# Performance work log

Hardware: AMD Instinct MI355X
Metric: run time of the kernel (lower is better)

## Reference

```python
import jax, jax.numpy as jnp
import numpy as np

B, N, P, D, NH, DFFN = 4, 1024, 128, 512, 8, 2048
DH = D // NH  # 64


def setup_inputs() -> dict:
    key = jax.random.key(0)
    ks = jax.random.split(key, 64)
    i = [0]
    def rn(shape, s=1.0):
        k = ks[i[0]]; i[0] += 1
        return jax.random.normal(k, shape, jnp.float32) * s
    w = 0.05  # weight init scale
    inp = {
        "H": rn((B, N, D)),
        "V": rn((B, N, 3, D)),
        "D_batch": rn((B, N, N)),
        "rbf_bias": rn((B, 1, N, N)),  # rbf_feat_batch[layer_idx]
        "prompt_feature": rn((B * P, D)),
        # self-attn params
        "Wq": rn((4 * D, D), w), "bq": jnp.zeros((4 * D,), jnp.float32),
        "Wk": rn((4 * D, D), w), "bk": jnp.zeros((4 * D,), jnp.float32),
        "Wv": rn((D, D), w), "bv": jnp.zeros((D,), jnp.float32),
        "Wvv": rn((D, D), w),
        "Wo": rn((D, D), w), "bo": jnp.zeros((D,), jnp.float32),
        "Wvo": rn((D, D), w),
        "ln1_g": jnp.ones((D,), jnp.float32), "ln1_b": jnp.zeros((D,), jnp.float32),
        # cross-attn params (nn.MultiheadAttention packed in_proj + out_proj, then scaler_o)
        "ca_in_w": rn((3 * D, D), w), "ca_in_b": jnp.zeros((3 * D,), jnp.float32),
        "ca_out_w": rn((D, D), w), "ca_out_b": jnp.zeros((D,), jnp.float32),
        "ca_so_w": rn((D, D), w), "ca_so_b": jnp.zeros((D,), jnp.float32),
        "ln2_g": jnp.ones((D,), jnp.float32), "ln2_b": jnp.zeros((D,), jnp.float32),
        # GVP-FFN params
        "ffn_lv": rn((2 * D, D), w),
        "ffn_w1": rn((DFFN, 2 * D), w), "ffn_b1": jnp.zeros((DFFN,), jnp.float32),
        "ffn_w2": rn((2 * D, DFFN), w), "ffn_b2": jnp.zeros((2 * D,), jnp.float32),
        "ln3_g": jnp.ones((D,), jnp.float32), "ln3_b": jnp.zeros((D,), jnp.float32),
        # key-validity mask [B,N]
        "H_mask": jax.random.randint(ks[60], (B, N), 0, 2).astype(jnp.int32),
    }
    return inp


def _ln(x, g, b):
    m = x.mean(-1, keepdims=True)
    v = ((x - m) ** 2).mean(-1, keepdims=True)
    return (x - m) / jnp.sqrt(v + 1e-5) * g + b


def _ept_layer(H, V, D_batch, rbf_bias, prompt_feature,
               Wq, bq, Wk, bk, Wv, bv, Wvv, Wo, bo, Wvo, ln1_g, ln1_b,
               ca_in_w, ca_in_b, ca_out_w, ca_out_b, ca_so_w, ca_so_b, ln2_g, ln2_b,
               ffn_lv, ffn_w1, ffn_b1, ffn_w2, ffn_b2, ln3_g, ln3_b, H_mask):
    factor = 0.5 / np.sqrt(DH)
    # ---- self-attn sublayer (pre-LN on H, residual on H and V) ----
    H0, V0 = H, V
    Hn = _ln(H, ln1_g, ln1_b)
    Hq = (Hn @ Wq.T + bq).reshape(B, N, NH, 4 * DH)
    Hk = (Hn @ Wk.T + bk).reshape(B, N, NH, 4 * DH)
    Hv = (Hn @ Wv.T + bv).reshape(B, N, NH, DH)
    # vector values: [B,N,3,D] -> [B,N,3,NH,DH] -> [B,N,NH,3,DH] -> [B,N,NH,3*DH]
    Vv = (V @ Wvv.T).reshape(B, N, 3, NH, DH).transpose(0, 1, 3, 2, 4).reshape(B, N, NH, 3 * DH)
    V_attn = jnp.concatenate([Hv, Vv], axis=-1)  # [B,N,NH,4*DH]
    bias = rbf_bias + D_batch[:, None]           # [B,1,N,N]
    bias = jnp.where(H_mask[:, None, None, :] == 0, -jnp.inf, bias)
    scores = jnp.einsum('bnhd,bmhd->bhnm', Hq, Hk) * factor + bias
    attn = jax.nn.softmax(scores, axis=-1)
    res = jnp.einsum('bhnm,bmhd->bnhd', attn, V_attn)  # [B,N,NH,4*DH]
    H_res = res[..., :DH].reshape(B, N, D)
    V_res = res[..., DH:].reshape(B, N, NH, 3, DH).transpose(0, 1, 3, 2, 4).reshape(B, N, 3, D)
    H = (H_res @ Wo.T + bo) + H0
    V = (V_res @ Wvo.T) + V0
    # ---- cross-attn sublayer (pre-LN, residual on H only) ----
    H0 = H
    Hn = _ln(H, ln2_g, ln2_b)
    prompt = prompt_feature.reshape(B, P, D)
    Wq_c, Wk_c, Wv_c = ca_in_w[:D], ca_in_w[D:2 * D], ca_in_w[2 * D:]
    bq_c, bk_c, bv_c = ca_in_b[:D], ca_in_b[D:2 * D], ca_in_b[2 * D:]
    q = (Hn @ Wq_c.T + bq_c).reshape(B, N, NH, DH)
    k = (prompt @ Wk_c.T + bk_c).reshape(B, P, NH, DH)
    v = (prompt @ Wv_c.T + bv_c).reshape(B, P, NH, DH)
    ca = jax.nn.softmax(jnp.einsum('bnhd,bphd->bhnp', q, k) / np.sqrt(DH), axis=-1)
    co = jnp.einsum('bhnp,bphd->bnhd', ca, v).reshape(B, N, D)
    co = co @ ca_out_w.T + ca_out_b
    H = (co @ ca_so_w.T + ca_so_b) + H0
    # ---- GVP-FFN sublayer (pre-LN on H, residual on H and V) ----
    H0, V0 = H, V
    Hn = _ln(H, ln3_g, ln3_b)
    Vp = V @ ffn_lv.T                  # [B,N,3,2D]
    V1, V2 = Vp[..., :D], Vp[..., D:]
    scaler = jnp.concatenate([Hn, jnp.linalg.norm(V1, axis=-2)], axis=-1)  # [B,N,2D]
    h1 = jax.nn.silu(scaler @ ffn_w1.T + ffn_b1)
    so = h1 @ ffn_w2.T + ffn_b2        # [B,N,2D]
    H_out, V_upd = so[..., :D], so[..., D:]
    H = H_out + H0
    V = V_upd[..., None, :] * V2 + V0  # vector_act == 'none'
    return H, V


def reference(H, V, D_batch, rbf_bias, prompt_feature,
              Wq, bq, Wk, bk, Wv, bv, Wvv, Wo, bo, Wvo, ln1_g, ln1_b,
              ca_in_w, ca_in_b, ca_out_w, ca_out_b, ca_so_w, ca_so_b, ln2_g, ln2_b,
              ffn_lv, ffn_w1, ffn_b1, ffn_w2, ffn_b2, ln3_g, ln3_b, H_mask):
    return _ept_layer(H, V, D_batch, rbf_bias, prompt_feature,
                      Wq, bq, Wk, bk, Wv, bv, Wvv, Wo, bo, Wvo, ln1_g, ln1_b,
                      ca_in_w, ca_in_b, ca_out_w, ca_out_b, ca_so_w, ca_so_b, ln2_g, ln2_b,
                      ffn_lv, ffn_w1, ffn_b1, ffn_w2, ffn_b2, ln3_g, ln3_b, H_mask)
```

## Files before the change

kernel.cpp:

```cpp
#include <hip/hip_runtime.h>
#include <cstdint>
#include <cstddef>

#define B_    4
#define N_    1024
#define P_    128
#define D_    512
#define NH_   8
#define QKVW  4608

typedef unsigned short ushort_t;
typedef short short8 __attribute__((ext_vector_type(8)));
typedef float f32x4 __attribute__((ext_vector_type(4)));
typedef ushort_t ushort4_t __attribute__((ext_vector_type(4)));

__device__ inline ushort_t f2bf(float f) {
  union { float fp; unsigned int u; } v; v.fp = f;
  unsigned int r = v.u + 0x7fffu + ((v.u >> 16) & 1u);
  return (ushort_t)(r >> 16);
}
__device__ inline float bf2f(ushort_t u) {
  union { unsigned int i; float f; } v; v.i = ((unsigned int)u) << 16;
  return v.f;
}

__device__ __forceinline__ void gll16(const ushort_t* g, ushort_t* l) {
  __builtin_amdgcn_global_load_lds(
      (const __attribute__((address_space(1))) void*)g,
      (__attribute__((address_space(3))) void*)l, 16, 0, 0);
}

__device__ inline void cast8(const float* __restrict__ s, ushort_t* __restrict__ d,
                             unsigned i) {
  const float* sp = s + (size_t)i * 8;
  short8 o;
#pragma unroll
  for (int j = 0; j < 8; ++j) o[j] = (short)f2bf(sp[j]);
  *(short8*)(d + (size_t)i * 8) = o;
}

__global__ __launch_bounds__(256) void cast_fused(
    const float* s0, ushort_t* d0,  const float* s1, ushort_t* d1,
    const float* s2, ushort_t* d2,  const float* s3, ushort_t* d3,
    const float* s4, ushort_t* d4,  const float* s5, ushort_t* d5,
    const float* s6, ushort_t* d6,  const float* s7, ushort_t* d7,
    const float* s8, ushort_t* d8,  const float* s9, ushort_t* d9,
    const float* s10, ushort_t* d10, const float* s11, ushort_t* d11,
    const float* s12, ushort_t* d12, const float* s13, ushort_t* d13)
{
  unsigned i = blockIdx.x * 256 + threadIdx.x;
#define SEG(s, d, n8) if (i < (n8)) { cast8(s, d, i); return; } i -= (n8);
  SEG(s0, d0, 131072u)
  SEG(s1, d1, 131072u)
  SEG(s2, d2, 32768u)
  SEG(s3, d3, 32768u)
  SEG(s4, d4, 32768u)
  SEG(s5, d5, 32768u)
  SEG(s6, d6, 98304u)
  SEG(s7, d7, 32768u)
  SEG(s8, d8, 32768u)
  SEG(s9, d9, 65536u)
  SEG(s10, d10, 262144u)
  SEG(s11, d11, 262144u)
  SEG(s12, d12, 32768u)
  SEG(s13, d13, 786432u)
#undef SEG
}

__global__ __launch_bounds__(256) void biasmerge3(
    const float* __restrict__ bq, const float* __restrict__ bk,
    const float* __restrict__ bv, float* __restrict__ o)
{
  int i = blockIdx.x * 256 + threadIdx.x;
  if (i >= 4608) return;
  o[i] = (i < 2048) ? bq[i] : (i < 4096) ? bk[i - 2048] : bv[i - 4096];
}

__global__ __launch_bounds__(256) void biascomb(const float* __restrict__ Db,
                                                const float* __restrict__ rbf,
                                                const int* __restrict__ mask,
                                                ushort_t* __restrict__ out)
{
  size_t i = (size_t)blockIdx.x * 256 + threadIdx.x;
  size_t e = i * 4;
  int b  = (int)(e >> 20);
  int m0 = (int)(e & 1023);
  float4 r = *(const float4*)(rbf + e);
  float4 d = *(const float4*)(Db + e);
  const int* mp = mask + b * 1024 + m0;
  ushort4_t o;
  o.x = f2bf(mp[0] ? r.x + d.x : -1e30f);
  o.y = f2bf(mp[1] ? r.y + d.y : -1e30f);
  o.z = f2bf(mp[2] ? r.z + d.z : -1e30f);
  o.w = f2bf(mp[3] ? r.w + d.w : -1e30f);
  *(ushort4_t*)(out + e) = o;
}

__global__ __launch_bounds__(256) void ln_kernel(
    const float* __restrict__ x, const float* __restrict__ g,
    const float* __restrict__ bb, ushort_t* __restrict__ y, int ostride)
{
  int row = blockIdx.x;
  int t = threadIdx.x;
  const float* xr = x + (size_t)row * D_;
  float a = xr[t], c = xr[t + 256];
  float s = a + c, sq = a * a + c * c;
#pragma unroll
  for (int off = 32; off >= 1; off >>= 1) {
    s  += __shfl_xor(s, off);
    sq += __shfl_xor(sq, off);
  }
  __shared__ float red[8];
  int w = t >> 6, lane = t & 63;
  if (lane == 0) { red[w] = s; red[4 + w] = sq; }
  __syncthreads();
  float st  = red[0] + red[1] + red[2] + red[3];
  float sqt = red[4] + red[5] + red[6] + red[7];
  float mean = st * (1.0f / D_);
  float var  = sqt * (1.0f / D_) - mean * mean;
  float inv  = rsqrtf(var + 1e-5f);
  y[(size_t)row * ostride + t]       = f2bf((a - mean) * inv * g[t] + bb[t]);
  y[(size_t)row * ostride + t + 256] = f2bf((c - mean) * inv * g[t + 256] + bb[t + 256]);
}

__global__ __launch_bounds__(256) void gemm_bf16(
    const ushort_t* __restrict__ A, const ushort_t* __restrict__ W,
    const float* __restrict__ bias, const float* __restrict__ res,
    float* __restrict__ Cf, ushort_t* __restrict__ Cb,
    int M, int N, int K, int flags)
{
  __shared__ __align__(16) ushort_t Al[128 * 32];
  __shared__ __align__(16) ushort_t Wl[128 * 32];
  const int t = threadIdx.x;
  const int wv = t >> 6, lane = t & 63, lr = lane & 15, lk = lane >> 4;
  const int wr = wv >> 1, wc = wv & 1;

  const int gx = gridDim.x;
  const int lid = blockIdx.y * gx + blockIdx.x;
  const int cpx = (gx * gridDim.y) >> 3;
  const int nlid = (lid & 7) * cpx + (lid >> 3);
  const size_t row0 = (size_t)(nlid / gx) * 128;
  const size_t col0 = (size_t)(nlid % gx) * 128;

  const int srow = 32 * wv + (lane >> 2);
  const int scol = (((lane & 3) ^ ((lane >> 3) & 3))) * 8;
  const ushort_t* ApG = A + (row0 + srow) * (size_t)K + scol;
  const ushort_t* WpG = W + (col0 + srow) * (size_t)K + scol;
  ushort_t* AlD = Al + (size_t)(32 * wv) * 32;
  ushort_t* WlD = Wl + (size_t)(32 * wv) * 32;
  const size_t K16 = (size_t)16 * K;

  f32x4 acc[4][4];
#pragma unroll
  for (int i = 0; i < 4; ++i)
#pragma unroll
    for (int j = 0; j < 4; ++j) acc[i][j] = f32x4{0.f, 0.f, 0.f, 0.f};

  const int sx = (lr >> 1) & 3;

  for (int k0 = 0; k0 < K; k0 += 32) {
    __syncthreads();
    gll16(ApG + k0,       AlD);
    gll16(ApG + k0 + K16, AlD + 512);
    gll16(WpG + k0,       WlD);
    gll16(WpG + k0 + K16, WlD + 512);
    __syncthreads();
    short8 af[4], bf[4];
#pragma unroll
    for (int i = 0; i < 4; ++i)
      af[i] = *(const short8*)&Al[(wr * 64 + i * 16 + lr) * 32 + ((lk ^ sx) << 3)];
#pragma unroll
    for (int j = 0; j < 4; ++j)
      bf[j] = *(const short8*)&Wl[(wc * 64 + j * 16 + lr) * 32 + ((lk ^ sx) << 3)];
#pragma unroll
    for (int i = 0; i < 4; ++i)
#pragma unroll
      for (int j = 0; j < 4; ++j)
        acc[i][j] = __builtin_amdgcn_mfma_f32_16x16x32_bf16(af[i], bf[j], acc[i][j], 0, 0, 0);
  }

  const int orow = wr * 64 + lk * 4, ocol = wc * 64 + lr;
#pragma unroll
  for (int i = 0; i < 4; ++i) {
#pragma unroll
    for (int j = 0; j < 4; ++j) {
      size_t colb = col0 + ocol + j * 16;
      float bv = (flags & 1) ? bias[colb] : 0.f;
#pragma unroll
      for (int r = 0; r < 4; ++r) {
        size_t rowg = row0 + orow + i * 16 + r;
        float v = acc[i][j][r] + bv;
        if (flags & 4) v = v / (1.f + __expf(-v));
        if (flags & 2) v += res[rowg * N + colb];
        if (flags & 8)  Cf[rowg * N + colb] = v;
        if (flags & 16) Cb[rowg * N + colb] = f2bf(v);
      }
    }
  }
}

__global__ __launch_bounds__(256) void gemm_bf16_sm(
    const ushort_t* __restrict__ A, const ushort_t* __restrict__ W,
    const float* __restrict__ bias, const float* __restrict__ res,
    float* __restrict__ Cf, ushort_t* __restrict__ Cb,
    int M, int N, int K, int flags)
{
  __shared__ __align__(16) ushort_t Al[64 * 32];
  __shared__ __align__(16) ushort_t Wl[128 * 32];
  const int t = threadIdx.x;
  const int wv = t >> 6, lane = t & 63, lr = lane & 15, lk = lane >> 4;
  const int wr = wv >> 1, wc = wv & 1;

  const int gx = gridDim.x;
  const int lid = blockIdx.y * gx + blockIdx.x;
  const int cpx = (gx * gridDim.y) >> 3;
  const int nlid = (lid & 7) * cpx + (lid >> 3);
  const size_t row0 = (size_t)(nlid / gx) * 64;
  const size_t col0 = (size_t)(nlid % gx) * 128;

  const int scol = (((lane & 3) ^ ((lane >> 3) & 3))) * 8;
  const int srowA = 16 * wv + (lane >> 2);
  const int srowW = 32 * wv + (lane >> 2);
  const ushort_t* ApG = A + (row0 + srowA) * (size_t)K + scol;
  const ushort_t* WpG = W + (col0 + srowW) * (size_t)K + scol;
  ushort_t* AlD = Al + (size_t)(16 * wv) * 32;
  ushort_t* WlD = Wl + (size_t)(32 * wv) * 32;
  const size_t K16 = (size_t)16 * K;

  f32x4 acc[2][4];
#pragma unroll
  for (int i = 0; i < 2; ++i)
#pragma unroll
    for (int j = 0; j < 4; ++j) acc[i][j] = f32x4{0.f, 0.f, 0.f, 0.f};

  const int sx = (lr >> 1) & 3;

  for (int k0 = 0; k0 < K; k0 += 32) {
    __syncthreads();
    gll16(ApG + k0,       AlD);
    gll16(WpG + k0,       WlD);
    gll16(WpG + k0 + K16, WlD + 512);
    __syncthreads();
    short8 af[2], bf[4];
#pragma unroll
    for (int i = 0; i < 2; ++i)
      af[i] = *(const short8*)&Al[(wr * 32 + i * 16 + lr) * 32 + ((lk ^ sx) << 3)];
#pragma unroll
    for (int j = 0; j < 4; ++j)
      bf[j] = *(const short8*)&Wl[(wc * 64 + j * 16 + lr) * 32 + ((lk ^ sx) << 3)];
#pragma unroll
    for (int i = 0; i < 2; ++i)
#pragma unroll
      for (int j = 0; j < 4; ++j)
        acc[i][j] = __builtin_amdgcn_mfma_f32_16x16x32_bf16(af[i], bf[j], acc[i][j], 0, 0, 0);
  }

  const int orow = wr * 32 + lk * 4, ocol = wc * 64 + lr;
#pragma unroll
  for (int i = 0; i < 2; ++i) {
#pragma unroll
    for (int j = 0; j < 4; ++j) {
      size_t colb = col0 + ocol + j * 16;
      float bv = (flags & 1) ? bias[colb] : 0.f;
#pragma unroll
      for (int r = 0; r < 4; ++r) {
        size_t rowg = row0 + orow + i * 16 + r;
        float v = acc[i][j][r] + bv;
        if (flags & 4) v = v / (1.f + __expf(-v));
        if (flags & 2) v += res[rowg * N + colb];
        if (flags & 8)  Cf[rowg * N + colb] = v;
        if (flags & 16) Cb[rowg * N + colb] = f2bf(v);
      }
    }
  }
}

__global__ __launch_bounds__(256) void vt_build(
    const ushort_t* __restrict__ QKVb, const ushort_t* __restrict__ VVTb,
    ushort_t* __restrict__ VT)
{
  const int bh = blockIdx.z, b = bh >> 3, h = bh & 7;
  const int n0 = blockIdx.x * 64, dt = blockIdx.y;
  __shared__ __align__(16) ushort_t tile[64][72];
  const int t = threadIdx.x;
  {
    int r = t >> 2, c0 = (t & 3) * 16;
    const ushort_t* src = (dt == 0)
      ? QKVb + ((size_t)(b * 1024 + n0 + r)) * QKVW + 4096 + h * 64 + c0
      : VVTb + (((size_t)(b * 1024 + n0 + r)) * 3 + (dt - 1)) * 512 + h * 64 + c0;
    *(short8*)&tile[r][c0]     = *(const short8*)src;
    *(short8*)&tile[r][c0 + 8] = *(const short8*)(src + 8);
  }
  __syncthreads();
  {
    int d = t >> 2, nc = (t & 3) * 16;
    short8 o0, o1;
#pragma unroll
    for (int i = 0; i < 8; ++i) { o0[i] = tile[nc + i][d]; o1[i] = tile[nc + 8 + i][d]; }
    ushort_t* dst = VT + ((size_t)bh * 256 + dt * 64 + d) * 1024 + n0 + nc;
    *(short8*)dst = o0;
    *(short8*)(dst + 8) = o1;
  }
}

__global__ __launch_bounds__(256) void attn_mfma(
    const ushort_t* __restrict__ QKg, const ushort_t* __restrict__ VTg,
    const ushort_t* __restrict__ biasb,
    ushort_t* __restrict__ HRESb, ushort_t* __restrict__ VRESb)
{
  const int blk = blockIdx.x;
  const int bi = blk >> 3;
  const int bh = (blk & 7) * 4 + (bi >> 4), b = bh >> 3, h = bh & 7;
  const int q0 = (bi & 15) * 64;
  const int t = threadIdx.x, w = t >> 6, lane = t & 63, lr = lane & 15, lk = lane >> 4;

  __shared__ __align__(16) ushort_t Kl[32][264];
  __shared__ __align__(16) ushort_t Vl[256][40];
  __shared__ __align__(16) ushort_t Pl[4][16][40];

  short8 qf[8];
  {
    const ushort_t* qb = QKg + ((size_t)(b * 1024 + q0 + w * 16 + lr)) * QKVW + h * 256;
#pragma unroll
    for (int s = 0; s < 8; ++s) qf[s] = *(const short8*)(qb + s * 32 + lk * 8);
  }
  f32x4 o[16];
#pragma unroll
  for (int i = 0; i < 16; ++i) o[i] = f32x4{0.f, 0.f, 0.f, 0.f};
  float mrow[4] = {-1e30f, -1e30f, -1e30f, -1e30f};
  float lsum[4] = {0.f, 0.f, 0.f, 0.f};
  const int qrow = q0 + w * 16 + lk * 4;

  const int krow = t >> 3, kc = (t & 7) * 32;
  const ushort_t* ksrc = QKg + ((size_t)(b * 1024 + krow)) * QKVW + 2048 + h * 256 + kc;
  const ushort_t* vsrc = VTg + ((size_t)bh * 256 + t) * 1024;
  const int vrot = (t >> 3) & 3;

  for (int k0 = 0; k0 < 1024; k0 += 32) {
    __syncthreads();
    {
      const ushort_t* ks = ksrc + (size_t)k0 * QKVW;
#pragma unroll
      for (int c = 0; c < 4; ++c)
        *(short8*)&Kl[krow][kc + c * 8] = *(const short8*)(ks + c * 8);
#pragma unroll
      for (int c = 0; c < 4; ++c) {
        int cc = (c + vrot) & 3;
        *(short8*)&Vl[t][cc * 8] = *(const short8*)(vsrc + k0 + cc * 8);
      }
    }
    __syncthreads();

    f32x4 s2[2];
    s2[0] = f32x4{0.f, 0.f, 0.f, 0.f};
    s2[1] = f32x4{0.f, 0.f, 0.f, 0.f};
    __builtin_amdgcn_s_setprio(1);
#pragma unroll
    for (int ks = 0; ks < 8; ++ks) {
#pragma unroll
      for (int j = 0; j < 2; ++j) {
        short8 kf = *(const short8*)&Kl[j * 16 + lr][ks * 32 + lk * 8];
        s2[j] = __builtin_amdgcn_mfma_f32_16x16x32_bf16(qf[ks], kf, s2[j], 0, 0, 0);
      }
    }
    __builtin_amdgcn_s_setprio(0);

    float sv[2][4];
    const ushort_t* bp = biasb + ((size_t)b << 20) + (size_t)qrow * 1024 + k0 + lr;
#pragma unroll
    for (int r = 0; r < 4; ++r) {
      sv[0][r] = s2[0][r] * 0.0625f + bf2f(bp[r * 1024]);
      sv[1][r] = s2[1][r] * 0.0625f + bf2f(bp[r * 1024 + 16]);
    }
    float pm[4], need = -1e30f;
#pragma unroll
    for (int r = 0; r < 4; ++r) {
      float m2 = fmaxf(sv[0][r], sv[1][r]);
      m2 = fmaxf(m2, __shfl_xor(m2, 1));
      m2 = fmaxf(m2, __shfl_xor(m2, 2));
      m2 = fmaxf(m2, __shfl_xor(m2, 4));
      m2 = fmaxf(m2, __shfl_xor(m2, 8));
      pm[r] = m2;
      need = fmaxf(need, m2 - mrow[r]);
    }
    if (!__all(need <= 8.f)) {
#pragma unroll
      for (int r = 0; r < 4; ++r) {
        float mn = fmaxf(mrow[r], pm[r]);
        float al = __expf(mrow[r] - mn);
        mrow[r] = mn;
        lsum[r] *= al;
#pragma unroll
        for (int d = 0; d < 16; ++d) o[d][r] *= al;
      }
    }
#pragma unroll
    for (int r = 0; r < 4; ++r) {
      float p0 = __expf(sv[0][r] - mrow[r]);
      float p1 = __expf(sv[1][r] - mrow[r]);
      float rs = p0 + p1;
      rs += __shfl_xor(rs, 1); rs += __shfl_xor(rs, 2);
      rs += __shfl_xor(rs, 4); rs += __shfl_xor(rs, 8);
      lsum[r] += rs;
      Pl[w][lk * 4 + r][lr]      = f2bf(p0);
      Pl[w][lk * 4 + r][16 + lr] = f2bf(p1);
    }
    short8 pf = *(const short8*)&Pl[w][lr][lk * 8];
    __builtin_amdgcn_s_setprio(1);
#pragma unroll
    for (int d = 0; d < 16; ++d) {
      short8 vf = *(const short8*)&Vl[d * 16 + lr][lk * 8];
      o[d] = __builtin_amdgcn_mfma_f32_16x16x32_bf16(pf, vf, o[d], 0, 0, 0);
    }
    __builtin_amdgcn_s_setprio(0);
  }

  float inv[4];
#pragma unroll
  for (int r = 0; r < 4; ++r) inv[r] = 1.f / lsum[r];
#pragma unroll
  for (int d = 0; d < 16; ++d) {
    int dcat = d * 16 + lr;
#pragma unroll
    for (int r = 0; r < 4; ++r) {
      float v = o[d][r] * inv[r];
      int n = qrow + r;
      if (dcat < 64)
        HRESb[((size_t)b * 1024 + n) * 512 + h * 64 + dcat] = f2bf(v);
      else {
        int c = (dcat - 64) >> 6, jj = (dcat - 64) & 63;
        VRESb[(((size_t)b * 1024 + n) * 3 + c) * 512 + h * 64 + jj] = f2bf(v);
      }
    }
  }
}

__global__ __launch_bounds__(256) void attn_cross_mfma(
    const ushort_t* __restrict__ Qb, const ushort_t* __restrict__ KVb,
    ushort_t* __restrict__ COb)
{
  const int bh = blockIdx.y, b = bh >> 3, h = bh & 7;
  const int q0 = blockIdx.x * 64;
  const int t = threadIdx.x, w = t >> 6, lane = t & 63, lr = lane & 15, lk = lane >> 4;

  __shared__ __align__(16) ushort_t Kl[128][72];
  __shared__ __align__(16) ushort_t Vt[64][136];
  __shared__ __align__(16) ushort_t Pl[4][16][136];

  {
    int p = t >> 1, c0 = (t & 1) * 32;
    const ushort_t* kp = KVb + ((size_t)b * 128 + p) * 1024 + h * 64 + c0;
#pragma unroll
    for (int i = 0; i < 4; ++i) {
      short8 kv = *(const short8*)(kp + i * 8);
      *(short8*)&Kl[p][c0 + i * 8] = kv;
      short8 vv = *(const short8*)(kp + 512 + i * 8);
#pragma unroll
      for (int jj = 0; jj < 8; ++jj) Vt[c0 + i * 8 + jj][p] = (ushort_t)vv[jj];
    }
  }
  __syncthreads();

  short8 qf[2];
  {
    const ushort_t* qp = Qb + ((size_t)b * 1024 + q0 + w * 16 + lr) * 512 + h * 64;
    qf[0] = *(const short8*)(qp + lk * 8);
    qf[1] = *(const short8*)(qp + 32 + lk * 8);
  }

  f32x4 s[8];
#pragma unroll
  for (int j = 0; j < 8; ++j) s[j] = f32x4{0.f, 0.f, 0.f, 0.f};
#pragma unroll
  for (int ks = 0; ks < 2; ++ks)
#pragma unroll
    for (int j = 0; j < 8; ++j) {
      short8 kf = *(const short8*)&Kl[j * 16 + lr][ks * 32 + lk * 8];
      s[j] = __builtin_amdgcn_mfma_f32_16x16x32_bf16(qf[ks], kf, s[j], 0, 0, 0);
    }

  float linv[4];
#pragma unroll
  for (int r = 0; r < 4; ++r) {
    float sc[8];
#pragma unroll
    for (int j = 0; j < 8; ++j) sc[j] = s[j][r] * 0.125f;
    float mx = sc[0];
#pragma unroll
    for (int j = 1; j < 8; ++j) mx = fmaxf(mx, sc[j]);
    mx = fmaxf(mx, __shfl_xor(mx, 1));
    mx = fmaxf(mx, __shfl_xor(mx, 2));
    mx = fmaxf(mx, __shfl_xor(mx, 4));
    mx = fmaxf(mx, __shfl_xor(mx, 8));
    float rs = 0.f;
#pragma unroll
    for (int j = 0; j < 8; ++j) {
      float p = __expf(sc[j] - mx);
      rs += p;
      Pl[w][lk * 4 + r][j * 16 + lr] = f2bf(p);
    }
    rs += __shfl_xor(rs, 1); rs += __shfl_xor(rs, 2);
    rs += __shfl_xor(rs, 4); rs += __shfl_xor(rs, 8);
    linv[r] = 1.f / rs;
  }
  __syncthreads();

  f32x4 o[4];
#pragma unroll
  for (int d = 0; d < 4; ++d) o[d] = f32x4{0.f, 0.f, 0.f, 0.f};
#pragma unroll
  for (int ks = 0; ks < 4; ++ks) {
    short8 pf = *(const short8*)&Pl[w][lr][ks * 32 + lk * 8];
#pragma unroll
    for (int d = 0; d < 4; ++d) {
      short8 vf = *(const short8*)&Vt[d * 16 + lr][ks * 32 + lk * 8];
      o[d] = __builtin_amdgcn_mfma_f32_16x16x32_bf16(pf, vf, o[d], 0, 0, 0);
    }
  }

#pragma unroll
  for (int d = 0; d < 4; ++d)
#pragma unroll
    for (int r = 0; r < 4; ++r) {
      int n = q0 + w * 16 + lk * 4 + r;
      COb[((size_t)b * 1024 + n) * 512 + h * 64 + d * 16 + lr] = f2bf(o[d][r] * linv[r]);
    }
}

__global__ __launch_bounds__(256) void vnorm_kernel(
    const ushort_t* __restrict__ Vp, ushort_t* __restrict__ scal)
{
  size_t i = (size_t)blockIdx.x * 256 + threadIdx.x;
  size_t bn = i >> 9; int d = (int)(i & 511);
  size_t base = bn * 3 * 1024 + d;
  float a = bf2f(Vp[base]);
  float b = bf2f(Vp[base + 1024]);
  float c = bf2f(Vp[base + 2048]);
  scal[bn * 1024 + 512 + d] = f2bf(sqrtf(a * a + b * b + c * c));
}

__global__ __launch_bounds__(256) void final_kernel(
    const float* __restrict__ so, const float* __restrict__ H2,
    const ushort_t* __restrict__ Vp, const float* __restrict__ Vnew,
    float* __restrict__ out)
{
  size_t i = (size_t)blockIdx.x * 256 + threadIdx.x;
  size_t bn = i >> 9; int d = (int)(i & 511);
  out[bn * 512 + d] = so[bn * 1024 + d] + H2[bn * 512 + d];
  float vu = so[bn * 1024 + 512 + d];
  float* outV = out + (size_t)B_ * N_ * D_;
#pragma unroll
  for (int c = 0; c < 3; ++c) {
    size_t vi = (bn * 3 + c) * 512 + d;
    outV[vi] = vu * bf2f(Vp[(bn * 3 + c) * 1024 + 512 + d]) + Vnew[vi];
  }
}

extern "C" void kernel_launch(void* const* d_in, const int* in_sizes, int n_in,
                              void* d_out, int out_size, void* d_ws, size_t ws_size,
                              hipStream_t stream)
{
  const float* H      = (const float*)d_in[0];
  const float* V      = (const float*)d_in[1];
  const float* Db     = (const float*)d_in[2];
  const float* rbf    = (const float*)d_in[3];
  const float* prompt = (const float*)d_in[4];
  const float* Wq  = (const float*)d_in[5];
  const float* bq  = (const float*)d_in[6];
  const float* Wk  = (const float*)d_in[7];
  const float* bk  = (const float*)d_in[8];
  const float* Wv  = (const float*)d_in[9];
  const float* bv  = (const float*)d_in[10];
  const float* Wvv = (const float*)d_in[11];
  const float* Wo  = (const float*)d_in[12];
  const float* bo  = (const float*)d_in[13];
  const float* Wvo = (const float*)d_in[14];
  const float* ln1g = (const float*)d_in[15];
  const float* ln1b = (const float*)d_in[16];
  const float* caw  = (const float*)d_in[17];
  const float* cab  = (const float*)d_in[18];
  const float* caow = (const float*)d_in[19];
  const float* caob = (const float*)d_in[20];
  const float* casw = (const float*)d_in[21];
  const float* casb = (const float*)d_in[22];
  const float* ln2g = (const float*)d_in[23];
  const float* ln2b = (const float*)d_in[24];
  const float* flv  = (const float*)d_in[25];
  const float* fw1  = (const float*)d_in[26];
  const float* fb1  = (const float*)d_in[27];
  const float* fw2  = (const float*)d_in[28];
  const float* fb2  = (const float*)d_in[29];
  const float* ln3g = (const float*)d_in[30];
  const float* ln3b = (const float*)d_in[31];
  const int*   mask = (const int*)d_in[32];

  char* wsb = (char*)d_ws;
  float* out = (float*)d_out;

#define HMB(x) ((size_t)(x) << 19)
  ushort_t* Wqkvb = (ushort_t*)(wsb + HMB(0));
  ushort_t* Wvvb  = (ushort_t*)(wsb + HMB(9));
  ushort_t* Wob   = (ushort_t*)(wsb + HMB(10));
  ushort_t* Wvob  = (ushort_t*)(wsb + HMB(11));
  ushort_t* cawb  = (ushort_t*)(wsb + HMB(12));
  ushort_t* caowb = (ushort_t*)(wsb + HMB(15));
  ushort_t* caswb = (ushort_t*)(wsb + HMB(16));
  ushort_t* flvb  = (ushort_t*)(wsb + HMB(17));
  ushort_t* fw1b  = (ushort_t*)(wsb + HMB(19));
  ushort_t* fw2b  = (ushort_t*)(wsb + HMB(27));
  ushort_t* promptb = (ushort_t*)(wsb + HMB(35));
  float*    BQKV  = (float*)   (wsb + HMB(36));
  ushort_t* HQKVb = (ushort_t*)(wsb + HMB(37));
  float*    VNEW  = (float*)   (wsb + HMB(37));
  ushort_t* VNEWb = (ushort_t*)(wsb + HMB(85));
  float*    SO    = (float*)   (wsb + HMB(85));
  ushort_t* VVTb  = (ushort_t*)(wsb + HMB(109));
  ushort_t* HN2b  = (ushort_t*)(wsb + HMB(109));
  ushort_t* QCb   = (ushort_t*)(wsb + HMB(117));
  ushort_t* KVCb  = (ushort_t*)(wsb + HMB(125));
  ushort_t* COb   = (ushort_t*)(wsb + HMB(127));
  ushort_t* Vb    = (ushort_t*)(wsb + HMB(133));
  ushort_t* HRESb = (ushort_t*)(wsb + HMB(133));
  ushort_t* CO2b  = (ushort_t*)(wsb + HMB(135));
  ushort_t* VRESb = (ushort_t*)(wsb + HMB(141));
  float*    H2    = (float*)   (wsb + HMB(143));
  ushort_t* HNb   = (ushort_t*)(wsb + HMB(157));
  ushort_t* VPb   = (ushort_t*)(wsb + HMB(159));
  ushort_t* VT    = (ushort_t*)(wsb + HMB(165));
  ushort_t* BIASCb= (ushort_t*)(wsb + HMB(197));
  float*    H1    = (float*)   (wsb + HMB(213));
  ushort_t* SCALb = (ushort_t*)(wsb + HMB(207));
  ushort_t* HH1b  = (ushort_t*)(wsb + HMB(223));

  cast_fused<<<7680, 256, 0, stream>>>(
      Wq, Wqkvb, Wk, Wqkvb + (size_t)2048 * 512, Wv, Wqkvb + (size_t)4096 * 512,
      Wvv, Wvvb, Wo, Wob, Wvo, Wvob, caw, cawb, caow, caowb, casw, caswb,
      flv, flvb, fw1, fw1b, fw2, fw2b, prompt, promptb, V, Vb);
  biasmerge3<<<18, 256, 0, stream>>>(bq, bk, bv, BQKV);
  biascomb<<<4096, 256, 0, stream>>>(Db, rbf, mask, BIASCb);
  ln_kernel<<<4096, 256, 0, stream>>>(H, ln1g, ln1b, HNb, 512);

  gemm_bf16<<<dim3(36, 32), 256, 0, stream>>>(HNb, Wqkvb, BQKV, nullptr, nullptr, HQKVb, 4096, 4608, 512, 1 | 16);
  gemm_bf16<<<dim3(4, 96), 256, 0, stream>>>(Vb, Wvvb, nullptr, nullptr, nullptr, VVTb, 12288, 512, 512, 16);

  vt_build<<<dim3(16, 4, 32), 256, 0, stream>>>(HQKVb, VVTb, VT);

  attn_mfma<<<512, 256, 0, stream>>>(HQKVb, VT, BIASCb, HRESb, VRESb);

  gemm_bf16_sm<<<dim3(4, 64), 256, 0, stream>>>(HRESb, Wob, bo, H, H1, nullptr, 4096, 512, 512, 1 | 2 | 8);
  gemm_bf16<<<dim3(4, 96), 256, 0, stream>>>(VRESb, Wvob, nullptr, V, VNEW, VNEWb, 12288, 512, 512, 2 | 8 | 16);

  ln_kernel<<<4096, 256, 0, stream>>>(H1, ln2g, ln2b, HN2b, 512);
  gemm_bf16_sm<<<dim3(4, 64), 256, 0, stream>>>(HN2b, cawb, cab, nullptr, nullptr, QCb, 4096, 512, 512, 1 | 16);
  gemm_bf16_sm<<<dim3(8, 8), 256, 0, stream>>>(promptb, cawb + 262144, cab + 512, nullptr, nullptr, KVCb, 512, 1024, 512, 1 | 16);

  attn_cross_mfma<<<dim3(16, 32), 256, 0, stream>>>(QCb, KVCb, COb);

  gemm_bf16_sm<<<dim3(4, 64), 256, 0, stream>>>(COb, caowb, caob, nullptr, nullptr, CO2b, 4096, 512, 512, 1 | 16);
  gemm_bf16_sm<<<dim3(4, 64), 256, 0, stream>>>(CO2b, caswb, casb, H1, H2, nullptr, 4096, 512, 512, 1 | 2 | 8);

  gemm_bf16<<<dim3(8, 96), 256, 0, stream>>>(VNEWb, flvb, nullptr, nullptr, nullptr, VPb, 12288, 1024, 512, 16);
  ln_kernel<<<4096, 256, 0, stream>>>(H2, ln3g, ln3b, SCALb, 1024);
  vnorm_kernel<<<8192, 256, 0, stream>>>(VPb, SCALb);

  gemm_bf16<<<dim3(16, 32), 256, 0, stream>>>(SCALb, fw1b, fb1, nullptr, nullptr, HH1b, 4096, 2048, 1024, 1 | 4 | 16);
  gemm_bf16_sm<<<dim3(8, 64), 256, 0, stream>>>(HH1b, fw2b, fb2, nullptr, SO, nullptr, 4096, 1024, 2048, 1 | 8);

  final_kernel<<<8192, 256, 0, stream>>>(SO, H2, VPb, VNEW, out);

  (void)in_sizes; (void)n_in; (void)out_size; (void)ws_size;
}
```

Before: 463.0 us.

## Split self-attention over key halves and merge partials in combine kernel

The self-attention kernel now splits the 1024 keys into two halves, launching twice as many blocks. Each block writes unnormalized bf16 partial outputs plus running max and sum, and a new combine kernel rescales and merges them into the H and V result buffers. The aim is more blocks in flight on a device with many CUs, since 512 blocks underfill it. The cost is an extra launch, partial-output memory traffic, and rounding partials to bf16 before the merge. Workspace buffers are also moved to fit the new intermediates.

```diff
diff --git a/kernel.cpp b/kernel.cpp
--- a/kernel.cpp
+++ b/kernel.cpp
@@ -306,12 +306,14 @@
 __global__ __launch_bounds__(256) void attn_mfma(
     const ushort_t* __restrict__ QKg, const ushort_t* __restrict__ VTg,
     const ushort_t* __restrict__ biasb,
-    ushort_t* __restrict__ HRESb, ushort_t* __restrict__ VRESb)
+    ushort_t* __restrict__ OPb, float* __restrict__ MLf)
 {
   const int blk = blockIdx.x;
   const int bi = blk >> 3;
-  const int bh = (blk & 7) * 4 + (bi >> 4), b = bh >> 3, h = bh & 7;
-  const int q0 = (bi & 15) * 64;
+  const int bh = (blk & 7) * 4 + (bi >> 5), b = bh >> 3, h = bh & 7;
+  const int qb = (bi >> 1) & 15, q0 = qb * 64;
+  const int s  = bi & 1, kbase = s * 512;
+  const int idx = (bh * 16 + qb) * 2 + s;
   const int t = threadIdx.x, w = t >> 6, lane = t & 63, lr = lane & 15, lk = lane >> 4;
 
   __shared__ __align__(16) ushort_t Kl[32][264];
@@ -320,9 +322,9 @@
 
   short8 qf[8];
   {
-    const ushort_t* qb = QKg + ((size_t)(b * 1024 + q0 + w * 16 + lr)) * QKVW + h * 256;
-#pragma unroll
-    for (int s = 0; s < 8; ++s) qf[s] = *(const short8*)(qb + s * 32 + lk * 8);
+    const ushort_t* qb_ = QKg + ((size_t)(b * 1024 + q0 + w * 16 + lr)) * QKVW + h * 256;
+#pragma unroll
+    for (int ss = 0; ss < 8; ++ss) qf[ss] = *(const short8*)(qb_ + ss * 32 + lk * 8);
   }
   f32x4 o[16];
 #pragma unroll
@@ -336,7 +338,7 @@
   const ushort_t* vsrc = VTg + ((size_t)bh * 256 + t) * 1024;
   const int vrot = (t >> 3) & 3;
 
-  for (int k0 = 0; k0 < 1024; k0 += 32) {
+  for (int k0 = kbase; k0 < kbase + 512; k0 += 32) {
     __syncthreads();
     {
       const ushort_t* ks = ksrc + (size_t)k0 * QKVW;
@@ -415,22 +417,57 @@
     __builtin_amdgcn_s_setprio(0);
   }
 
-  float inv[4];
-#pragma unroll
-  for (int r = 0; r < 4; ++r) inv[r] = 1.f / lsum[r];
-#pragma unroll
-  for (int d = 0; d < 16; ++d) {
-    int dcat = d * 16 + lr;
+  const size_t opbase = (size_t)idx * 16384 + (size_t)(w * 16 + lk * 4) * 256;
+#pragma unroll
+  for (int d = 0; d < 16; ++d)
+#pragma unroll
+    for (int r = 0; r < 4; ++r)
+      OPb[opbase + (size_t)r * 256 + d * 16 + lr] = f2bf(o[d][r]);
+  if (lr == 0) {
 #pragma unroll
     for (int r = 0; r < 4; ++r) {
-      float v = o[d][r] * inv[r];
-      int n = qrow + r;
-      if (dcat < 64)
-        HRESb[((size_t)b * 1024 + n) * 512 + h * 64 + dcat] = f2bf(v);
-      else {
-        int c = (dcat - 64) >> 6, jj = (dcat - 64) & 63;
-        VRESb[(((size_t)b * 1024 + n) * 3 + c) * 512 + h * 64 + jj] = f2bf(v);
-      }
+      int row = w * 16 + lk * 4 + r;
+      MLf[(size_t)idx * 128 + row]      = mrow[r];
+      MLf[(size_t)idx * 128 + 64 + row] = lsum[r];
+    }
+  }
+}
+
+__global__ __launch_bounds__(256) void attn_combine(
+    const ushort_t* __restrict__ OPb, const float* __restrict__ MLf,
+    ushort_t* __restrict__ HRESb, ushort_t* __restrict__ VRESb)
+{
+  const int blk = blockIdx.x;
+  const int bh = blk >> 4, b = bh >> 3, h = bh & 7;
+  const int t = threadIdx.x;
+  const int row = t >> 2, dc0 = (t & 3) * 64;
+  const int n = (blk & 15) * 64 + row;
+
+  const size_t i0 = (size_t)(blk * 2) * 128, i1 = i0 + 128;
+  float m0 = MLf[i0 + row], l0 = MLf[i0 + 64 + row];
+  float m1 = MLf[i1 + row], l1 = MLf[i1 + 64 + row];
+  float ms = fmaxf(m0, m1);
+  float a0 = __expf(m0 - ms), a1 = __expf(m1 - ms);
+  float inv = 1.f / (l0 * a0 + l1 * a1);
+
+  const ushort_t* p0 = OPb + (size_t)(blk * 2) * 16384 + (size_t)row * 256 + dc0;
+  const ushort_t* p1 = p0 + 16384;
+  ushort_t* dstH = HRESb + ((size_t)b * 1024 + n) * 512 + h * 64;
+#pragma unroll
+  for (int c8 = 0; c8 < 8; ++c8) {
+    short8 v0 = *(const short8*)(p0 + c8 * 8);
+    short8 v1 = *(const short8*)(p1 + c8 * 8);
+    short8 ov;
+#pragma unroll
+    for (int j = 0; j < 8; ++j)
+      ov[j] = (short)f2bf((bf2f((ushort_t)v0[j]) * a0 + bf2f((ushort_t)v1[j]) * a1) * inv);
+    int dcat = dc0 + c8 * 8;
+    if (dc0 == 0) {
+      *(short8*)(dstH + dcat) = ov;
+    } else {
+      int c = (dc0 >> 6) - 1;
+      ushort_t* dstV = VRESb + (((size_t)b * 1024 + n) * 3 + c) * 512 + h * 64;
+      *(short8*)(dstV + (dcat - (c + 1) * 64)) = ov;
     }
   }
 }
@@ -614,23 +651,25 @@
   float*    VNEW  = (float*)   (wsb + HMB(37));
   ushort_t* VNEWb = (ushort_t*)(wsb + HMB(85));
   float*    SO    = (float*)   (wsb + HMB(85));
+  ushort_t* OPb   = (ushort_t*)(wsb + HMB(109));
+  float*    MLf   = (float*)   (wsb + HMB(173));
   ushort_t* VVTb  = (ushort_t*)(wsb + HMB(109));
   ushort_t* HN2b  = (ushort_t*)(wsb + HMB(109));
   ushort_t* QCb   = (ushort_t*)(wsb + HMB(117));
   ushort_t* KVCb  = (ushort_t*)(wsb + HMB(125));
   ushort_t* COb   = (ushort_t*)(wsb + HMB(127));
   ushort_t* Vb    = (ushort_t*)(wsb + HMB(133));
-  ushort_t* HRESb = (ushort_t*)(wsb + HMB(133));
   ushort_t* CO2b  = (ushort_t*)(wsb + HMB(135));
-  ushort_t* VRESb = (ushort_t*)(wsb + HMB(141));
   float*    H2    = (float*)   (wsb + HMB(143));
   ushort_t* HNb   = (ushort_t*)(wsb + HMB(157));
   ushort_t* VPb   = (ushort_t*)(wsb + HMB(159));
-  ushort_t* VT    = (ushort_t*)(wsb + HMB(165));
   ushort_t* BIASCb= (ushort_t*)(wsb + HMB(197));
+  ushort_t* SCALb = (ushort_t*)(wsb + HMB(207));
+  ushort_t* VT    = (ushort_t*)(wsb + HMB(213));
   float*    H1    = (float*)   (wsb + HMB(213));
-  ushort_t* SCALb = (ushort_t*)(wsb + HMB(207));
+  ushort_t* HRESb = (ushort_t*)(wsb + HMB(229));
   ushort_t* HH1b  = (ushort_t*)(wsb + HMB(223));
+  ushort_t* VRESb = (ushort_t*)(wsb + HMB(245));
 
   cast_fused<<<7680, 256, 0, stream>>>(
       Wq, Wqkvb, Wk, Wqkvb + (size_t)2048 * 512, Wv, Wqkvb + (size_t)4096 * 512,
@@ -645,7 +684,8 @@
 
   vt_build<<<dim3(16, 4, 32), 256, 0, stream>>>(HQKVb, VVTb, VT);
 
-  attn_mfma<<<512, 256, 0, stream>>>(HQKVb, VT, BIASCb, HRESb, VRESb);
+  attn_mfma<<<1024, 256, 0, stream>>>(HQKVb, VT, BIASCb, OPb, MLf);
+  attn_combine<<<512, 256, 0, stream>>>(OPb, MLf, HRESb, VRESb);
 
   gemm_bf16_sm<<<dim3(4, 64), 256, 0, stream>>>(HRESb, Wob, bo, H, H1, nullptr, 4096, 512, 512, 1 | 2 | 8);
   gemm_bf16<<<dim3(4, 96), 256, 0, stream>>>(VRESb, Wvob, nullptr, V, VNEW, VNEWb, 12288, 512, 512, 2 | 8 | 16);
```

After: 521.1 us. 12.5% more time.
